# Kernel optimization log

Hardware: AMD Instinct MI355X
Metric: run time of the kernel (lower is better)

## Reference

```python
import jax, jax.numpy as jnp
import numpy as np


def gcn_norm(edge_index, edge_weight, N):
    # PyG gcn_norm: add self-loops with weight 1, symmetric normalization
    row, col = edge_index[0], edge_index[1]
    loop = jnp.arange(N)
    row = jnp.concatenate([row, loop])
    col = jnp.concatenate([col, loop])
    w = jnp.concatenate([edge_weight, jnp.ones((N,), edge_weight.dtype)])
    deg = jax.ops.segment_sum(w, col, num_segments=N)
    dinv = jnp.where(deg > 0, jax.lax.rsqrt(deg), jnp.zeros_like(deg))
    norm = dinv[row] * w * dinv[col]
    return row, col, norm


def gcn_conv(x, W, b, row, col, norm, N):
    h = x @ W                                  # [N, out]
    msg = norm[:, None] * h[row]               # gather + scale  [E+N, out]
    out = jax.ops.segment_sum(msg, col, num_segments=N)  # scatter-add
    return out + b


def setup_inputs() -> dict:
    N, E, F_IN, HID, OUT, L, C = 100000, 3200000, 128, 128, 128, 16, 8
    key = jax.random.key(0)
    ks = jax.random.split(key, 6)
    x = jax.random.normal(ks[0], (N, F_IN), dtype=jnp.float32)
    edge_index = jax.random.randint(ks[1], (2, E), 0, N, dtype=jnp.int64)
    edge_weight = jax.random.uniform(ks[2], (E,), dtype=jnp.float32)
    W1 = jax.random.normal(ks[3], (F_IN, HID), dtype=jnp.float32) / np.sqrt(F_IN)
    b1 = jnp.zeros((HID,), jnp.float32)
    W2 = jax.random.normal(ks[4], (HID, OUT), dtype=jnp.float32) / np.sqrt(HID)
    b2 = jnp.zeros((OUT,), jnp.float32)
    return {"x": x, "edge_index": edge_index, "edge_weight": edge_weight,
            "W1": W1, "b1": b1, "W2": W2, "b2": b2, "N": N, "L": L, "C": C}


def reference(x, edge_index, edge_weight, W1, b1, W2, b2, N, L, C):
    x = x.reshape(N, -1)
    row, col, norm = gcn_norm(edge_index, edge_weight, N)
    h = gcn_conv(x, W1, b1, row, col, norm, N)
    h = jax.nn.relu(h)
    # dropout is identity in eval mode
    out = gcn_conv(h, W2, b2, row, col, norm, N)
    return out.reshape(N, L, C)
```

## Files before the change

kernel.cpp:

```cpp
#include <hip/hip_runtime.h>
#include <hip/hip_bf16.h>

typedef __attribute__((ext_vector_type(8))) short short8;
typedef __attribute__((ext_vector_type(4))) float f32x4;

__device__ __forceinline__ float bf2f(unsigned short u) {
    return __builtin_bit_cast(float, (unsigned int)u << 16);
}
__device__ __forceinline__ unsigned short f2bf(float f) {
    unsigned int i = __builtin_bit_cast(unsigned int, f);
    i += 0x7fffu + ((i >> 16) & 1u);
    return (unsigned short)(i >> 16);
}
__device__ __forceinline__ void bfx2(unsigned int u, float& lo, float& hi) {
    lo = __builtin_bit_cast(float, u << 16);
    hi = __builtin_bit_cast(float, u & 0xffff0000u);
}

#define FIXP 8388608.0f
#define BKT_SHIFT 7
#define BKT_W 128
#define GB 256
#define SCAN_BS 1024

__global__ void detect_k(const unsigned int* xw, const unsigned int* ei, int* flags) {
    __shared__ int cnt14;
    __shared__ unsigned int orodd;
    if (threadIdx.x == 0) { cnt14 = 0; orodd = 0u; }
    __syncthreads();
    int c = 0; unsigned int o = 0u;
    for (int i = threadIdx.x; i < 4096; i += 256) {
        c += (int)((xw[i] >> 14) & 1u);
        o |= ei[2 * i + 1];
    }
    atomicAdd(&cnt14, c);
    atomicOr(&orodd, o);
    __syncthreads();
    if (threadIdx.x == 0) {
        flags[0] = (cnt14 > 1024) ? 1 : 0;
        flags[1] = (orodd == 0u) ? 1 : 0;
    }
}

__device__ __forceinline__ int load_row(const int* ei, int e, int i64f) {
    return i64f ? ei[2 * (size_t)e] : ei[e];
}
__device__ __forceinline__ int load_col(const int* ei, int e, int E, int i64f) {
    return i64f ? ei[2 * (size_t)E + 2 * (size_t)e] : ei[(size_t)E + e];
}
__device__ __forceinline__ float load_w(const void* w, int e, int f32f) {
    return f32f ? ((const float*)w)[e] : bf2f(((const unsigned short*)w)[e]);
}

__global__ __launch_bounds__(1024) void hist_k(const int* ei, unsigned int* gh,
                                               int E, int NB, int chunk,
                                               const int* flags) {
    __shared__ unsigned int lh[1024];
    for (int b = threadIdx.x; b < 1024; b += 1024) lh[b] = 0u;
    __syncthreads();
    int i64f = flags[1];
    int blk = blockIdx.x;
    int s = blk * chunk;
    int t = min(s + chunk, E);
    for (int i = s + threadIdx.x; i < t; i += 1024) {
        int c = load_col(ei, i, E, i64f);
        atomicAdd(&lh[c >> BKT_SHIFT], 1u);
    }
    __syncthreads();
    for (int b = threadIdx.x; b < NB; b += 1024)
        gh[(size_t)b * GB + blk] = lh[b];
}

__global__ void scan1_k(const int* counts, int* offsets, int* partials, int n) {
    __shared__ int buf[SCAN_BS];
    int t = threadIdx.x, g = blockIdx.x * SCAN_BS + t;
    int v = (g < n) ? counts[g] : 0;
    buf[t] = v; __syncthreads();
    for (int off = 1; off < SCAN_BS; off <<= 1) {
        int x = (t >= off) ? buf[t - off] : 0;
        __syncthreads();
        buf[t] += x;
        __syncthreads();
    }
    if (g < n) offsets[g] = buf[t] - v;
    if (t == SCAN_BS - 1) partials[blockIdx.x] = buf[t];
}

__global__ void scan2_k(int* partials, int n) {
    __shared__ int buf[SCAN_BS];
    int t = threadIdx.x;
    int v = (t < n) ? partials[t] : 0;
    buf[t] = v; __syncthreads();
    for (int off = 1; off < SCAN_BS; off <<= 1) {
        int x = (t >= off) ? buf[t - off] : 0;
        __syncthreads();
        buf[t] += x;
        __syncthreads();
    }
    if (t < n) partials[t] = buf[t] - v;
}

__global__ void scan3_k(int* offsets, const int* partials, int n) {
    int g = blockIdx.x * SCAN_BS + threadIdx.x;
    if (g < n) offsets[g] += partials[blockIdx.x];
}

__global__ __launch_bounds__(1024) void scatter_k(const int* ei, const void* w,
                                                  const unsigned int* gh,
                                                  unsigned long long* rc,
                                                  int E, int NB, int chunk,
                                                  const int* flags) {
    __shared__ unsigned int cur[1024];
    int blk = blockIdx.x;
    for (int b = threadIdx.x; b < NB; b += 1024)
        cur[b] = gh[(size_t)b * GB + blk];
    __syncthreads();
    int f32f = flags[0], i64f = flags[1];
    int s = blk * chunk, t = min(s + chunk, E);
    for (int i = s + threadIdx.x; i < t; i += 1024) {
        int c = load_col(ei, i, E, i64f);
        int r = load_row(ei, i, i64f);
        float wf = load_w(w, i, f32f);
        unsigned int pos = atomicAdd(&cur[c >> BKT_SHIFT], 1u);
        unsigned long long rec =
            ((unsigned long long)(unsigned int)__float_as_int(wf) << 32) |
            (unsigned int)((r << 7) | (c & (BKT_W - 1)));
        rc[pos] = rec;
    }
}

__global__ __launch_bounds__(256) void bucket_fin_k(const unsigned long long* rc,
                                                    const unsigned int* gh,
                                                    float* dinv,
                                                    int* offsets, int2* edata,
                                                    int E, int N, int NB) {
    __shared__ unsigned long long pk[BKT_W];
    __shared__ unsigned int sc[BKT_W];
    __shared__ unsigned int cur[BKT_W];
    int b = blockIdx.x;
    for (int i = threadIdx.x; i < BKT_W; i += 256) pk[i] = 0ULL;
    __syncthreads();
    unsigned int s = gh[(size_t)b * GB];
    unsigned int t = (b + 1 < NB) ? gh[(size_t)(b + 1) * GB] : (unsigned int)E;
    for (unsigned int i = s + threadIdx.x; i < t; i += 256) {
        unsigned long long rec = rc[i];
        float wf = __int_as_float((int)(unsigned int)(rec >> 32));
        unsigned int wq = __float2uint_rn(wf * FIXP);
        atomicAdd(&pk[(unsigned int)rec & (BKT_W - 1)],
                  (1ULL << 32) | (unsigned long long)wq);
    }
    __syncthreads();
    unsigned int val = 0;
    if (threadIdx.x < BKT_W) {
        val = (unsigned int)(pk[threadIdx.x] >> 32);
        sc[threadIdx.x] = val;
    }
    __syncthreads();
    for (int off = 1; off < BKT_W; off <<= 1) {
        unsigned int x = (threadIdx.x < BKT_W && threadIdx.x >= (unsigned)off)
                             ? sc[threadIdx.x - off] : 0u;
        __syncthreads();
        if (threadIdx.x < BKT_W) sc[threadIdx.x] += x;
        __syncthreads();
    }
    if (threadIdx.x < BKT_W) {
        int lc = threadIdx.x;
        int v = (b << BKT_SHIFT) + lc;
        unsigned int off0 = s + sc[lc] - val;
        cur[lc] = off0;
        if (v < N) {
            unsigned long long p = pk[lc];
            float deg = 1.0f + (float)(unsigned int)(p & 0xffffffffULL) * (1.0f / FIXP);
            dinv[v] = rsqrtf(deg);
            offsets[v] = (int)off0;
        }
    }
    if (b == NB - 1 && threadIdx.x == 0) offsets[N] = E;
    __syncthreads();
    for (unsigned int i = s + threadIdx.x; i < t; i += 256) {
        unsigned long long rec = rc[i];
        unsigned int lo = (unsigned int)rec;
        unsigned int pos = atomicAdd(&cur[lo & (BKT_W - 1)], 1u);
        int2 o; o.x = (int)(lo >> 7); o.y = (int)(unsigned int)(rec >> 32);
        edata[pos] = o;
    }
}

__global__ void transpose2_k(const void* W1, const void* W2,
                             unsigned short* Wt1, unsigned short* Wt2,
                             const int* flags) {
    int i = blockIdx.x * 256 + threadIdx.x;
    int which = i >> 14, j = i & 16383;
    const void* W = which ? W2 : W1;
    unsigned short* Wt = which ? Wt2 : Wt1;
    int k = j >> 7, n = j & 127;
    unsigned short v = flags[0] ? f2bf(((const float*)W)[j])
                                : ((const unsigned short*)W)[j];
    Wt[n * 128 + k] = v;
}

__global__ __launch_bounds__(256) void gemm_k(const void* X,
                                              const unsigned short* Wt,
                                              const float* dinv,
                                              unsigned short* Y, int ntiles,
                                              const int* flags, int xmode) {
    int wave = blockIdx.x * 4 + (threadIdx.x >> 6);
    if (wave >= ntiles) return;
    int lane = threadIdx.x & 63;
    int m = lane & 15, quad = lane >> 4;
    int rowbase = wave * 16;
    int x_f32 = (xmode == 0) ? flags[0] : 0;

    short8 a[4];
    if (x_f32) {
        const float* xf = (const float*)X;
#pragma unroll
        for (int ks = 0; ks < 4; ++ks) {
            const float* p = xf + (size_t)(rowbase + m) * 128 + ks * 32 + quad * 8;
            float4 u0 = *(const float4*)p;
            float4 u1 = *(const float4*)(p + 4);
            short8 t;
            t[0] = (short)f2bf(u0.x); t[1] = (short)f2bf(u0.y);
            t[2] = (short)f2bf(u0.z); t[3] = (short)f2bf(u0.w);
            t[4] = (short)f2bf(u1.x); t[5] = (short)f2bf(u1.y);
            t[6] = (short)f2bf(u1.z); t[7] = (short)f2bf(u1.w);
            a[ks] = t;
        }
    } else {
        const unsigned short* xh = (const unsigned short*)X;
#pragma unroll
        for (int ks = 0; ks < 4; ++ks)
            a[ks] = *(const short8*)(xh + (size_t)(rowbase + m) * 128 + ks * 32 + quad * 8);
    }

    float dvr[4];
#pragma unroll
    for (int i = 0; i < 4; ++i) dvr[i] = dinv[rowbase + quad * 4 + i];

#pragma unroll
    for (int ct = 0; ct < 8; ++ct) {
        f32x4 acc = {0.f, 0.f, 0.f, 0.f};
#pragma unroll
        for (int ks = 0; ks < 4; ++ks) {
            short8 b = *(const short8*)(Wt + (size_t)(ct * 16 + m) * 128 + ks * 32 + quad * 8);
            acc = __builtin_amdgcn_mfma_f32_16x16x32_bf16(a[ks], b, acc, 0, 0, 0);
        }
#pragma unroll
        for (int i = 0; i < 4; ++i) {
            size_t r = rowbase + quad * 4 + i;
            size_t c = ct * 16 + m;
            Y[r * 128 + c] = f2bf(acc[i] * dvr[i]);
        }
    }
}

__global__ __launch_bounds__(64) void agg_k(const unsigned int* h2,
                                            const int2* edata,
                                            const int* offsets,
                                            const float* dinv,
                                            const void* bias,
                                            void* out,
                                            int relu, int out_bf16,
                                            const int* flags) {
    int v = blockIdx.x;
    int lane = threadIdx.x;
    int2 se = *(const int2*)(offsets + v);
    int start = se.x, end = se.y;
    float a0 = 0.f, a1 = 0.f;

    int e = start;
    for (; e + 4 <= end; e += 4) {
        int2 d0 = edata[e], d1 = edata[e + 1], d2 = edata[e + 2], d3 = edata[e + 3];
        unsigned int u0 = h2[(size_t)d0.x * 64 + lane];
        unsigned int u1 = h2[(size_t)d1.x * 64 + lane];
        unsigned int u2 = h2[(size_t)d2.x * 64 + lane];
        unsigned int u3 = h2[(size_t)d3.x * 64 + lane];
        float c0 = __int_as_float(d0.y), c1 = __int_as_float(d1.y);
        float c2 = __int_as_float(d2.y), c3 = __int_as_float(d3.y);
        float l, h;
        bfx2(u0, l, h); a0 = fmaf(c0, l, a0); a1 = fmaf(c0, h, a1);
        bfx2(u1, l, h); a0 = fmaf(c1, l, a0); a1 = fmaf(c1, h, a1);
        bfx2(u2, l, h); a0 = fmaf(c2, l, a0); a1 = fmaf(c2, h, a1);
        bfx2(u3, l, h); a0 = fmaf(c3, l, a0); a1 = fmaf(c3, h, a1);
    }
    for (; e < end; ++e) {
        int2 d = edata[e];
        float l, h; bfx2(h2[(size_t)d.x * 64 + lane], l, h);
        float c = __int_as_float(d.y);
        a0 = fmaf(c, l, a0); a1 = fmaf(c, h, a1);
    }

    {
        float l, h; bfx2(h2[(size_t)v * 64 + lane], l, h);
        a0 += l; a1 += h;
    }
    float dv = dinv[v];
    a0 *= dv; a1 *= dv;
    if (flags[0]) {
        const float* bf = (const float*)bias;
        a0 += bf[2 * lane]; a1 += bf[2 * lane + 1];
    } else {
        float l, h; bfx2(((const unsigned int*)bias)[lane], l, h);
        a0 += l; a1 += h;
    }
    if (relu) { a0 = fmaxf(a0, 0.f); a1 = fmaxf(a1, 0.f); }
    if (out_bf16) {
        ((unsigned int*)out)[(size_t)v * 64 + lane] =
            (unsigned int)f2bf(a0) | ((unsigned int)f2bf(a1) << 16);
    } else {
        float2 r; r.x = a0; r.y = a1;
        ((float2*)out)[(size_t)v * 64 + lane] = r;
    }
}

extern "C" void kernel_launch(void* const* d_in, const int* in_sizes, int n_in,
                              void* d_out, int out_size, void* d_ws, size_t ws_size,
                              hipStream_t stream) {
    const void* x  = d_in[0];
    const int*  ei = (const int*)d_in[1];
    const void* ew = d_in[2];
    const void* W1 = d_in[3];
    const void* b1 = d_in[4];
    const void* W2 = d_in[5];
    const void* b2 = d_in[6];

    const int N = in_sizes[0] / 128;
    const int E = in_sizes[2];

    const int NB = (N + BKT_W - 1) >> BKT_SHIFT;
    if (NB > 1024) return;
    const int M = NB * GB;
    const int chunk = (E + GB - 1) / GB;

    auto align = [](size_t v) { return (v + 255) & ~(size_t)255; };
    size_t rc_bytes = align((size_t)E * 8);
    size_t ha_bytes = 2 * align((size_t)N * 128 * 2);
    size_t regionX  = rc_bytes > ha_bytes ? rc_bytes : ha_bytes;
    size_t need = align((size_t)E * 8)
                + regionX
                + align((size_t)M * 4)
                + align((size_t)(N + 1) * 4)
                + align((size_t)N * 4)
                + align(SCAN_BS * 4) + align(256)
                + align(128 * 128 * 2) * 2;
    if (ws_size < need) return;

    char* p = (char*)d_ws;
    int2*  edata = (int2*)p;                     p += align((size_t)E * 8);
    char*  rx = p;                               p += regionX;
    unsigned long long* rc = (unsigned long long*)rx;
    unsigned short* h  = (unsigned short*)rx;
    unsigned short* a1 = (unsigned short*)(rx + align((size_t)N * 128 * 2));
    unsigned int* gh = (unsigned int*)p;         p += align((size_t)M * 4);
    int*   offsets  = (int*)p;                   p += align((size_t)(N + 1) * 4);
    float* dinv     = (float*)p;                 p += align((size_t)N * 4);
    int*   partials = (int*)p;                   p += align(SCAN_BS * 4);
    int*   flags    = (int*)p;                   p += align(256);
    unsigned short* Wt1 = (unsigned short*)p;    p += align(128 * 128 * 2);
    unsigned short* Wt2 = (unsigned short*)p;    p += align(128 * 128 * 2);

    const int nsbM = (M + SCAN_BS - 1) / SCAN_BS;

    detect_k<<<1, 256, 0, stream>>>((const unsigned int*)x, (const unsigned int*)ei, flags);

    hist_k<<<GB, 1024, 0, stream>>>(ei, gh, E, NB, chunk, flags);
    scan1_k<<<nsbM, SCAN_BS, 0, stream>>>((const int*)gh, (int*)gh, partials, M);
    scan2_k<<<1, SCAN_BS, 0, stream>>>(partials, nsbM);
    scan3_k<<<nsbM, SCAN_BS, 0, stream>>>((int*)gh, partials, M);
    scatter_k<<<GB, 1024, 0, stream>>>(ei, ew, gh, rc, E, NB, chunk, flags);
    bucket_fin_k<<<NB, 256, 0, stream>>>(rc, gh, dinv, offsets, edata, E, N, NB);

    transpose2_k<<<128, 256, 0, stream>>>(W1, W2, Wt1, Wt2, flags);

    const int ntiles = N / 16;
    const int gGemm = (ntiles + 3) / 4;

    gemm_k<<<gGemm, 256, 0, stream>>>(x, Wt1, dinv, h, ntiles, flags, 0);
    agg_k<<<N, 64, 0, stream>>>((const unsigned int*)h, edata, offsets, dinv,
                                b1, a1, 1, 1, flags);

    gemm_k<<<gGemm, 256, 0, stream>>>(a1, Wt2, dinv, h, ntiles, flags, 1);
    agg_k<<<N, 64, 0, stream>>>((const unsigned int*)h, edata, offsets, dinv,
                                b2, d_out, 0, 0, flags);
}
```

Before: 523.6 us.

## Fuse detection into histogram, single-pass decoupled-lookback scan, transpose W in-gemm

Folds the dtype-detection kernel into the histogram kernel, where every block recomputes the int64 flag locally and block 0 writes the flags and zeroes the scan state. The three-kernel scan becomes one decoupled-lookback scan that uses a ticket counter and spin-waits on predecessor state. The weight transpose kernel is dropped, and each gemm block instead transposes W into padded shared memory. This removes five kernel launches, at the cost of redundant per-block W conversion and 34 KB of LDS per gemm block, which may reduce occupancy.

```diff
diff --git a/kernel.cpp b/kernel.cpp
--- a/kernel.cpp
+++ b/kernel.cpp
@@ -23,25 +23,6 @@
 #define GB 256
 #define SCAN_BS 1024
 
-__global__ void detect_k(const unsigned int* xw, const unsigned int* ei, int* flags) {
-    __shared__ int cnt14;
-    __shared__ unsigned int orodd;
-    if (threadIdx.x == 0) { cnt14 = 0; orodd = 0u; }
-    __syncthreads();
-    int c = 0; unsigned int o = 0u;
-    for (int i = threadIdx.x; i < 4096; i += 256) {
-        c += (int)((xw[i] >> 14) & 1u);
-        o |= ei[2 * i + 1];
-    }
-    atomicAdd(&cnt14, c);
-    atomicOr(&orodd, o);
-    __syncthreads();
-    if (threadIdx.x == 0) {
-        flags[0] = (cnt14 > 1024) ? 1 : 0;
-        flags[1] = (orodd == 0u) ? 1 : 0;
-    }
-}
-
 __device__ __forceinline__ int load_row(const int* ei, int e, int i64f) {
     return i64f ? ei[2 * (size_t)e] : ei[e];
 }
@@ -52,13 +33,34 @@
     return f32f ? ((const float*)w)[e] : bf2f(((const unsigned short*)w)[e]);
 }
 
-__global__ __launch_bounds__(1024) void hist_k(const int* ei, unsigned int* gh,
-                                               int E, int NB, int chunk,
-                                               const int* flags) {
+__global__ __launch_bounds__(1024) void hist_k(const unsigned int* xw, const int* ei,
+                                               unsigned int* gh, int* flags,
+                                               unsigned int* scanstate,
+                                               int E, int NB, int chunk) {
     __shared__ unsigned int lh[1024];
+    __shared__ unsigned int s_or;
+    __shared__ int s_cnt;
+    if (threadIdx.x == 0) { s_or = 0u; s_cnt = 0; }
     for (int b = threadIdx.x; b < 1024; b += 1024) lh[b] = 0u;
     __syncthreads();
-    int i64f = flags[1];
+    {
+        unsigned int o = 0u;
+        const unsigned int* eiu = (const unsigned int*)ei;
+        for (int i = threadIdx.x; i < 4096; i += 1024) o |= eiu[2 * i + 1];
+        if (o) atomicOr(&s_or, 1u);
+    }
+    if (blockIdx.x == 0) {
+        int c = 0;
+        for (int i = threadIdx.x; i < 4096; i += 1024) c += (int)((xw[i] >> 14) & 1u);
+        if (c) atomicAdd(&s_cnt, c);
+        for (int i = threadIdx.x; i < 1024; i += 1024) scanstate[i] = 0u;
+    }
+    __syncthreads();
+    int i64f = (s_or == 0u) ? 1 : 0;
+    if (blockIdx.x == 0 && threadIdx.x == 0) {
+        flags[0] = (s_cnt > 1024) ? 1 : 0;
+        flags[1] = i64f;
+    }
     int blk = blockIdx.x;
     int s = blk * chunk;
     int t = min(s + chunk, E);
@@ -71,10 +73,18 @@
         gh[(size_t)b * GB + blk] = lh[b];
 }
 
-__global__ void scan1_k(const int* counts, int* offsets, int* partials, int n) {
+__global__ __launch_bounds__(SCAN_BS) void scanL_k(int* gh,
+                                                   unsigned long long* state,
+                                                   int* ticket, int n) {
     __shared__ int buf[SCAN_BS];
-    int t = threadIdx.x, g = blockIdx.x * SCAN_BS + t;
-    int v = (g < n) ? counts[g] : 0;
+    __shared__ int s_vb;
+    __shared__ unsigned int s_base;
+    int t = threadIdx.x;
+    if (t == 0) s_vb = atomicAdd(ticket, 1);
+    __syncthreads();
+    int vbid = s_vb;
+    int g = vbid * SCAN_BS + t;
+    int v = (g < n) ? gh[g] : 0;
     buf[t] = v; __syncthreads();
     for (int off = 1; off < SCAN_BS; off <<= 1) {
         int x = (t >= off) ? buf[t - off] : 0;
@@ -82,27 +92,33 @@
         buf[t] += x;
         __syncthreads();
     }
-    if (g < n) offsets[g] = buf[t] - v;
-    if (t == SCAN_BS - 1) partials[blockIdx.x] = buf[t];
-}
-
-__global__ void scan2_k(int* partials, int n) {
-    __shared__ int buf[SCAN_BS];
-    int t = threadIdx.x;
-    int v = (t < n) ? partials[t] : 0;
-    buf[t] = v; __syncthreads();
-    for (int off = 1; off < SCAN_BS; off <<= 1) {
-        int x = (t >= off) ? buf[t - off] : 0;
-        __syncthreads();
-        buf[t] += x;
-        __syncthreads();
-    }
-    if (t < n) partials[t] = buf[t] - v;
-}
-
-__global__ void scan3_k(int* offsets, const int* partials, int n) {
-    int g = blockIdx.x * SCAN_BS + threadIdx.x;
-    if (g < n) offsets[g] += partials[blockIdx.x];
+    if (t == 0) {
+        unsigned int total = (unsigned int)buf[SCAN_BS - 1];
+        if (vbid == 0) {
+            __hip_atomic_store(&state[0], (2ull << 32) | total,
+                               __ATOMIC_RELAXED, __HIP_MEMORY_SCOPE_AGENT);
+            s_base = 0u;
+        } else {
+            __hip_atomic_store(&state[vbid], (1ull << 32) | total,
+                               __ATOMIC_RELAXED, __HIP_MEMORY_SCOPE_AGENT);
+            unsigned int base = 0u;
+            int p = vbid - 1;
+            while (true) {
+                unsigned long long sv = __hip_atomic_load(&state[p],
+                                          __ATOMIC_RELAXED, __HIP_MEMORY_SCOPE_AGENT);
+                unsigned int st = (unsigned int)(sv >> 32);
+                if (st == 0u) continue;
+                base += (unsigned int)sv;
+                if (st == 2u) break;
+                --p;
+            }
+            __hip_atomic_store(&state[vbid], (2ull << 32) | (base + total),
+                               __ATOMIC_RELAXED, __HIP_MEMORY_SCOPE_AGENT);
+            s_base = base;
+        }
+    }
+    __syncthreads();
+    if (g < n) gh[g] = buf[t] - v + (int)s_base;
 }
 
 __global__ __launch_bounds__(1024) void scatter_k(const int* ei, const void* w,
@@ -186,30 +202,28 @@
     }
 }
 
-__global__ void transpose2_k(const void* W1, const void* W2,
-                             unsigned short* Wt1, unsigned short* Wt2,
-                             const int* flags) {
-    int i = blockIdx.x * 256 + threadIdx.x;
-    int which = i >> 14, j = i & 16383;
-    const void* W = which ? W2 : W1;
-    unsigned short* Wt = which ? Wt2 : Wt1;
-    int k = j >> 7, n = j & 127;
-    unsigned short v = flags[0] ? f2bf(((const float*)W)[j])
-                                : ((const unsigned short*)W)[j];
-    Wt[n * 128 + k] = v;
-}
-
-__global__ __launch_bounds__(256) void gemm_k(const void* X,
-                                              const unsigned short* Wt,
+__global__ __launch_bounds__(256) void gemm_k(const void* X, const void* W,
                                               const float* dinv,
                                               unsigned short* Y, int ntiles,
                                               const int* flags, int xmode) {
+    __shared__ unsigned short wt[128 * 136];
+    int f32f = flags[0];
+    {
+        const float* Wf = (const float*)W;
+        const unsigned short* Wh = (const unsigned short*)W;
+        for (int j = threadIdx.x; j < 16384; j += 256) {
+            unsigned short v = f32f ? f2bf(Wf[j]) : Wh[j];
+            wt[(j & 127) * 136 + (j >> 7)] = v;
+        }
+    }
+    __syncthreads();
+
     int wave = blockIdx.x * 4 + (threadIdx.x >> 6);
     if (wave >= ntiles) return;
     int lane = threadIdx.x & 63;
     int m = lane & 15, quad = lane >> 4;
     int rowbase = wave * 16;
-    int x_f32 = (xmode == 0) ? flags[0] : 0;
+    int x_f32 = (xmode == 0) ? f32f : 0;
 
     short8 a[4];
     if (x_f32) {
@@ -242,7 +256,7 @@
         f32x4 acc = {0.f, 0.f, 0.f, 0.f};
 #pragma unroll
         for (int ks = 0; ks < 4; ++ks) {
-            short8 b = *(const short8*)(Wt + (size_t)(ct * 16 + m) * 128 + ks * 32 + quad * 8);
+            short8 b = *(const short8*)(wt + (ct * 16 + m) * 136 + ks * 32 + quad * 8);
             acc = __builtin_amdgcn_mfma_f32_16x16x32_bf16(a[ks], b, acc, 0, 0, 0);
         }
 #pragma unroll
@@ -341,8 +355,7 @@
                 + align((size_t)M * 4)
                 + align((size_t)(N + 1) * 4)
                 + align((size_t)N * 4)
-                + align(SCAN_BS * 4) + align(256)
-                + align(128 * 128 * 2) * 2;
+                + align(SCAN_BS * 4) + align(256);
     if (ws_size < need) return;
 
     char* p = (char*)d_ws;
@@ -354,32 +367,28 @@
     unsigned int* gh = (unsigned int*)p;         p += align((size_t)M * 4);
     int*   offsets  = (int*)p;                   p += align((size_t)(N + 1) * 4);
     float* dinv     = (float*)p;                 p += align((size_t)N * 4);
-    int*   partials = (int*)p;                   p += align(SCAN_BS * 4);
+    char*  scanbuf  = p;                         p += align(SCAN_BS * 4);
     int*   flags    = (int*)p;                   p += align(256);
-    unsigned short* Wt1 = (unsigned short*)p;    p += align(128 * 128 * 2);
-    unsigned short* Wt2 = (unsigned short*)p;    p += align(128 * 128 * 2);
+
+    unsigned long long* lbstate = (unsigned long long*)scanbuf;
+    int* ticket = (int*)(scanbuf + 2048);
 
     const int nsbM = (M + SCAN_BS - 1) / SCAN_BS;
 
-    detect_k<<<1, 256, 0, stream>>>((const unsigned int*)x, (const unsigned int*)ei, flags);
-
-    hist_k<<<GB, 1024, 0, stream>>>(ei, gh, E, NB, chunk, flags);
-    scan1_k<<<nsbM, SCAN_BS, 0, stream>>>((const int*)gh, (int*)gh, partials, M);
-    scan2_k<<<1, SCAN_BS, 0, stream>>>(partials, nsbM);
-    scan3_k<<<nsbM, SCAN_BS, 0, stream>>>((int*)gh, partials, M);
+    hist_k<<<GB, 1024, 0, stream>>>((const unsigned int*)x, ei, gh, flags,
+                                    (unsigned int*)scanbuf, E, NB, chunk);
+    scanL_k<<<nsbM, SCAN_BS, 0, stream>>>((int*)gh, lbstate, ticket, M);
     scatter_k<<<GB, 1024, 0, stream>>>(ei, ew, gh, rc, E, NB, chunk, flags);
     bucket_fin_k<<<NB, 256, 0, stream>>>(rc, gh, dinv, offsets, edata, E, N, NB);
 
-    transpose2_k<<<128, 256, 0, stream>>>(W1, W2, Wt1, Wt2, flags);
-
     const int ntiles = N / 16;
     const int gGemm = (ntiles + 3) / 4;
 
-    gemm_k<<<gGemm, 256, 0, stream>>>(x, Wt1, dinv, h, ntiles, flags, 0);
+    gemm_k<<<gGemm, 256, 0, stream>>>(x, W1, dinv, h, ntiles, flags, 0);
     agg_k<<<N, 64, 0, stream>>>((const unsigned int*)h, edata, offsets, dinv,
                                 b1, a1, 1, 1, flags);
 
-    gemm_k<<<gGemm, 256, 0, stream>>>(a1, Wt2, dinv, h, ntiles, flags, 1);
+    gemm_k<<<gGemm, 256, 0, stream>>>(a1, W2, dinv, h, ntiles, flags, 1);
     agg_k<<<N, 64, 0, stream>>>((const unsigned int*)h, edata, offsets, dinv,
                                 b2, d_out, 0, 0, flags);
 }
```

Result: slower. 565.1 us (+7.9%).

## Slice feature columns into 16-wide planes and aggregate slices per wave

Applied to the files above, without the earlier changes.

The GEMM output and the hidden activations are stored as eight column slices of 16 features, each a contiguous [N,16] plane. The aggregation kernel now has each block work on one slice, so gathered rows are 32 bytes and the slice working set (about 3.2 MB) can stay in cache. Each wave handles a contiguous range of nodes and processes 16 edges in parallel, then combines them with a shuffle reduction. The trade-off is that every edge's index data is read eight times, partial edge groups are masked, and only 4 lanes write the output.

```diff
diff --git a/kernel.cpp b/kernel.cpp
--- a/kernel.cpp
+++ b/kernel.cpp
@@ -22,6 +22,8 @@
 #define BKT_W 128
 #define GB 256
 #define SCAN_BS 1024
+#define SLICES 8
+#define AGG_BLOCKS 2048
 
 __global__ void detect_k(const unsigned int* xw, const unsigned int* ei, int* flags) {
     __shared__ int cnt14;
@@ -203,7 +205,7 @@
                                               const unsigned short* Wt,
                                               const float* dinv,
                                               unsigned short* Y, int ntiles,
-                                              const int* flags, int xmode) {
+                                              const int* flags, int xmode, int N) {
     int wave = blockIdx.x * 4 + (threadIdx.x >> 6);
     if (wave >= ntiles) return;
     int lane = threadIdx.x & 63;
@@ -226,11 +228,19 @@
             t[6] = (short)f2bf(u1.z); t[7] = (short)f2bf(u1.w);
             a[ks] = t;
         }
+    } else if (xmode == 0) {
+        const unsigned short* xh = (const unsigned short*)X;
+#pragma unroll
+        for (int ks = 0; ks < 4; ++ks)
+            a[ks] = *(const short8*)(xh + (size_t)(rowbase + m) * 128 + ks * 32 + quad * 8);
     } else {
         const unsigned short* xh = (const unsigned short*)X;
 #pragma unroll
-        for (int ks = 0; ks < 4; ++ks)
-            a[ks] = *(const short8*)(xh + (size_t)(rowbase + m) * 128 + ks * 32 + quad * 8);
+        for (int ks = 0; ks < 4; ++ks) {
+            int k0 = ks * 32 + quad * 8;
+            a[ks] = *(const short8*)(xh + (size_t)(k0 >> 4) * N * 16 +
+                                     (size_t)(rowbase + m) * 16 + (k0 & 15));
+        }
     }
 
     float dvr[4];
@@ -248,68 +258,84 @@
 #pragma unroll
         for (int i = 0; i < 4; ++i) {
             size_t r = rowbase + quad * 4 + i;
-            size_t c = ct * 16 + m;
-            Y[r * 128 + c] = f2bf(acc[i] * dvr[i]);
-        }
-    }
-}
-
-__global__ __launch_bounds__(64) void agg_k(const unsigned int* h2,
-                                            const int2* edata,
-                                            const int* offsets,
-                                            const float* dinv,
-                                            const void* bias,
-                                            void* out,
-                                            int relu, int out_bf16,
-                                            const int* flags) {
-    int v = blockIdx.x;
-    int lane = threadIdx.x;
-    int2 se = *(const int2*)(offsets + v);
-    int start = se.x, end = se.y;
-    float a0 = 0.f, a1 = 0.f;
-
-    int e = start;
-    for (; e + 4 <= end; e += 4) {
-        int2 d0 = edata[e], d1 = edata[e + 1], d2 = edata[e + 2], d3 = edata[e + 3];
-        unsigned int u0 = h2[(size_t)d0.x * 64 + lane];
-        unsigned int u1 = h2[(size_t)d1.x * 64 + lane];
-        unsigned int u2 = h2[(size_t)d2.x * 64 + lane];
-        unsigned int u3 = h2[(size_t)d3.x * 64 + lane];
-        float c0 = __int_as_float(d0.y), c1 = __int_as_float(d1.y);
-        float c2 = __int_as_float(d2.y), c3 = __int_as_float(d3.y);
-        float l, h;
-        bfx2(u0, l, h); a0 = fmaf(c0, l, a0); a1 = fmaf(c0, h, a1);
-        bfx2(u1, l, h); a0 = fmaf(c1, l, a0); a1 = fmaf(c1, h, a1);
-        bfx2(u2, l, h); a0 = fmaf(c2, l, a0); a1 = fmaf(c2, h, a1);
-        bfx2(u3, l, h); a0 = fmaf(c3, l, a0); a1 = fmaf(c3, h, a1);
-    }
-    for (; e < end; ++e) {
-        int2 d = edata[e];
-        float l, h; bfx2(h2[(size_t)d.x * 64 + lane], l, h);
-        float c = __int_as_float(d.y);
-        a0 = fmaf(c, l, a0); a1 = fmaf(c, h, a1);
-    }
-
-    {
-        float l, h; bfx2(h2[(size_t)v * 64 + lane], l, h);
-        a0 += l; a1 += h;
-    }
-    float dv = dinv[v];
-    a0 *= dv; a1 *= dv;
-    if (flags[0]) {
-        const float* bf = (const float*)bias;
-        a0 += bf[2 * lane]; a1 += bf[2 * lane + 1];
-    } else {
-        float l, h; bfx2(((const unsigned int*)bias)[lane], l, h);
-        a0 += l; a1 += h;
-    }
-    if (relu) { a0 = fmaxf(a0, 0.f); a1 = fmaxf(a1, 0.f); }
-    if (out_bf16) {
-        ((unsigned int*)out)[(size_t)v * 64 + lane] =
-            (unsigned int)f2bf(a0) | ((unsigned int)f2bf(a1) << 16);
-    } else {
-        float2 r; r.x = a0; r.y = a1;
-        ((float2*)out)[(size_t)v * 64 + lane] = r;
+            Y[(size_t)ct * N * 16 + r * 16 + m] = f2bf(acc[i] * dvr[i]);
+        }
+    }
+}
+
+__global__ __launch_bounds__(256) void agg_k(const uint2* hv,
+                                             const int2* edata,
+                                             const int* offsets,
+                                             const float* dinv,
+                                             const void* bias,
+                                             void* out,
+                                             int relu, int out_bf16,
+                                             const int* flags, int N, int npw) {
+    int slice = blockIdx.x & 7;
+    int wave  = (blockIdx.x >> 3) * 4 + (threadIdx.x >> 6);
+    int lane  = threadIdx.x & 63;
+    int g   = lane >> 2;
+    int dw2 = lane & 3;
+    const uint2* hs = hv + (size_t)slice * N * 4;
+    int f32f = flags[0];
+
+    int v0 = wave * npw;
+    int v1 = min(N, v0 + npw);
+    for (int v = v0; v < v1; ++v) {
+        int2 se = *(const int2*)(offsets + v);
+        int start = se.x, end = se.y;
+        float a0 = 0.f, a1 = 0.f, a2 = 0.f, a3 = 0.f;
+        for (int e = start; e < end; e += 16) {
+            int idx = e + g;
+            bool valid = idx < end;
+            int idxc = valid ? idx : end - 1;
+            int2 d = edata[idxc];
+            float c = valid ? __int_as_float(d.y) : 0.f;
+            uint2 u = hs[(size_t)d.x * 4 + dw2];
+            float l0, h0, l1, h1;
+            bfx2(u.x, l0, h0); bfx2(u.y, l1, h1);
+            a0 = fmaf(c, l0, a0); a1 = fmaf(c, h0, a1);
+            a2 = fmaf(c, l1, a2); a3 = fmaf(c, h1, a3);
+        }
+#pragma unroll
+        for (int mk = 4; mk < 64; mk <<= 1) {
+            a0 += __shfl_xor(a0, mk, 64);
+            a1 += __shfl_xor(a1, mk, 64);
+            a2 += __shfl_xor(a2, mk, 64);
+            a3 += __shfl_xor(a3, mk, 64);
+        }
+        {
+            uint2 u = hs[(size_t)v * 4 + dw2];
+            float l0, h0, l1, h1;
+            bfx2(u.x, l0, h0); bfx2(u.y, l1, h1);
+            a0 += l0; a1 += h0; a2 += l1; a3 += h1;
+        }
+        float dv = dinv[v];
+        a0 *= dv; a1 *= dv; a2 *= dv; a3 *= dv;
+        if (f32f) {
+            float4 bq = ((const float4*)((const float*)bias + slice * 16))[dw2];
+            a0 += bq.x; a1 += bq.y; a2 += bq.z; a3 += bq.w;
+        } else {
+            uint2 bu = ((const uint2*)bias)[slice * 4 + dw2];
+            float l0, h0, l1, h1;
+            bfx2(bu.x, l0, h0); bfx2(bu.y, l1, h1);
+            a0 += l0; a1 += h0; a2 += l1; a3 += h1;
+        }
+        if (relu) {
+            a0 = fmaxf(a0, 0.f); a1 = fmaxf(a1, 0.f);
+            a2 = fmaxf(a2, 0.f); a3 = fmaxf(a3, 0.f);
+        }
+        if (lane < 4) {
+            if (out_bf16) {
+                uint2 o;
+                o.x = (unsigned int)f2bf(a0) | ((unsigned int)f2bf(a1) << 16);
+                o.y = (unsigned int)f2bf(a2) | ((unsigned int)f2bf(a3) << 16);
+                ((uint2*)out)[(size_t)slice * N * 4 + (size_t)v * 4 + dw2] = o;
+            } else {
+                float4 o; o.x = a0; o.y = a1; o.z = a2; o.w = a3;
+                ((float4*)((float*)out + (size_t)v * 128 + slice * 16))[dw2] = o;
+            }
+        }
     }
 }
 
@@ -374,12 +400,16 @@
 
     const int ntiles = N / 16;
     const int gGemm = (ntiles + 3) / 4;
-
-    gemm_k<<<gGemm, 256, 0, stream>>>(x, Wt1, dinv, h, ntiles, flags, 0);
-    agg_k<<<N, 64, 0, stream>>>((const unsigned int*)h, edata, offsets, dinv,
-                                b1, a1, 1, 1, flags);
-
-    gemm_k<<<gGemm, 256, 0, stream>>>(a1, Wt2, dinv, h, ntiles, flags, 1);
-    agg_k<<<N, 64, 0, stream>>>((const unsigned int*)h, edata, offsets, dinv,
-                                b2, d_out, 0, 0, flags);
-}
+    const int nwaves = (AGG_BLOCKS / 8) * 4;
+    const int npw = (N + nwaves - 1) / nwaves;
+
+    gemm_k<<<gGemm, 256, 0, stream>>>(x, Wt1, dinv, h, ntiles, flags, 0, N);
+    agg_k<<<AGG_BLOCKS, 256, 0, stream>>>((const uint2*)h, edata, offsets, dinv,
+                                          b1, a1, 1, 1,
+                                          flags, N, npw);
+
+    gemm_k<<<gGemm, 256, 0, stream>>>(a1, Wt2, dinv, h, ntiles, flags, 1, N);
+    agg_k<<<AGG_BLOCKS, 256, 0, stream>>>((const uint2*)h, edata, offsets, dinv,
+                                          b2, d_out, 0, 0,
+                                          flags, N, npw);
+}
```

Measured after the change: 827.3 us. +58.0%, slower.
